# Performance work log

Hardware: AMD Instinct MI355X
Metric: run time of the kernel (lower is better)

## Reference

```python
import jax, jax.numpy as jnp
import numpy as np
from jax import lax

B, A, H, W = 64, 8, 64, 128
T_EXP = 32
ACTION_HORIZON = 64
DS = 1.0          # reward_cfg['ds']
TEMPERATURE = 0.1 # policy_kwargs['temperature'], method='sharpen'
FOV_HALF_ANGLE_DEG = 35.0
FOV_MAX_RANGE = 100


def _build_buffers():
    # per-action 3x3 one-hot transition kernels: weight 1.0 at 'center' cell,
    # 0.0 at left/right cells (as in MaxEntIRL.__init__ with policy_method='pp')
    center = [[2, 2], [2, 1], [2, 0], [1, 2], [1, 0], [0, 2], [0, 1], [0, 0]]
    tp = np.zeros((A, 1, 3, 3), np.float32)
    for i, (r, c) in enumerate(center):
        tp[i, 0, r, c] = 1.0
    # trapezoidal FOV mask built on a (2H, W) grid, then cropped to first H rows
    rows = np.arange(2 * H, dtype=np.float32)[:, None]
    cols = np.arange(W, dtype=np.float32)[None, :]
    half = np.tan(np.deg2rad(FOV_HALF_ANGLE_DEG)) * rows
    mask = ((np.abs(cols - (W - 1) / 2.0) <= half) & (rows <= FOV_MAX_RANGE))
    fov = mask.astype(np.float32)[:H][None, None]  # (1,1,H,W)
    dyn = np.array([[-1, -1], [-1, 0], [-1, 1], [0, -1],
                    [0, 1], [1, -1], [1, 0], [1, 1]], np.int32)
    return jnp.asarray(tp), jnp.asarray(fov), jnp.asarray(dyn)


def setup_inputs() -> dict:
    key = jax.random.key(0)
    k1, k2 = jax.random.split(key)
    policy = jax.random.normal(k1, (B, A, H, W), jnp.float32)
    # expert SE(2)-like poses; only [:, :, :2, 2] translations are read.
    # Scale to [0,100) so grid cells spread over the map before clamping.
    expert = jax.random.uniform(k2, (B, T_EXP, 3, 3), jnp.float32) * 100.0
    tp, fov, dyn = _build_buffers()
    return {"policy": policy, "expert": expert, "transition_probs": tp,
            "fov_mask": fov, "dynamics": dyn, "action_horizon": ACTION_HORIZON}


def reference(policy, expert, transition_probs, fov_mask, dynamics, action_horizon):
    Bn, An, Hn, Wn = policy.shape
    n_states = Hn * Wn
    barange = jnp.arange(Bn)

    # expert poses -> clamped grid cells  (S: (B, T, 2))
    S = jnp.floor_divide(expert[:, :, :2, 2], DS).astype(jnp.int32)
    S = jnp.stack([jnp.clip(S[..., 0], 0, Hn - 1),
                   jnp.clip(S[..., 1], 0, Wn - 1)], axis=-1)

    # earliest pose inside FOV (argmax of bool gives first True, else 0)
    mask2d = fov_mask[0, 0]
    in_fov = mask2d[S[..., 0], S[..., 1]] > 0  # (B, T)
    idx0 = jnp.argmax(in_fov, axis=1)
    S0c = S[barange, idx0]     # (B, 2) start cell
    S1c = S[:, -1]             # (B, 2) terminal cell
    S0 = S0c[:, 0] * Wn + S0c[:, 1]
    S1 = S1c[:, 0] * Wn + S1c[:, 1]

    # sharpen policy over action dim (stable softmax with temperature)
    logits = (policy - jnp.max(policy, axis=1, keepdims=True)) / TEMPERATURE
    policy_2d = jax.nn.softmax(logits, axis=1)  # (B, A, H, W)

    mu0 = jnp.zeros((Bn, n_states), jnp.float32).at[barange, S0].set(1.0)

    def step(carry, _):
        prev, total = carry
        # zero_terminal_state: kill visitation mass at the terminal cell
        prev_z = prev.at[barange, S1].set(0.0)
        pm = policy_2d * prev_z.reshape(Bn, 1, Hn, Wn)  # (B, A, H, W)
        new = lax.conv_general_dilated(
            pm, transition_probs, window_strides=(1, 1),
            padding=[(1, 1), (1, 1)],
            dimension_numbers=("NCHW", "OIHW", "NCHW"),
            feature_group_count=An)
        new = jnp.sum(new, axis=1).reshape(Bn, n_states)
        return (new, total + prev_z), None

    (last, total), _ = lax.scan(step, (mu0, jnp.zeros_like(mu0)),
                                None, length=action_horizon - 1)
    mu = (total + last).reshape(Bn, Hn, Wn)

    # greedy rollout (torch runs this under no_grad)
    policy_flat = policy.reshape(Bn, An, n_states)
    most_likely_action = jnp.argmax(policy_flat, axis=1)  # (B, n_states)
    most_likely_action = lax.stop_gradient(most_likely_action)

    def roll(St, _):
        a = most_likely_action[barange, St]
        coord = jnp.stack([St // Wn, St % Wn], axis=1) + dynamics[a]
        coord = jnp.stack([jnp.clip(coord[:, 0], 0, Hn - 1),
                           jnp.clip(coord[:, 1], 0, Wn - 1)], axis=1)
        return coord[:, 0] * Wn + coord[:, 1], coord

    _, coords = lax.scan(roll, S0, None, length=action_horizon - 1)  # (T-1,B,2)
    states = jnp.concatenate([S0c[None].astype(coords.dtype), coords],
                             axis=0).transpose(1, 0, 2)  # (B, T, 2)
    bidx = jnp.broadcast_to(barange[:, None], (Bn, action_horizon))
    states_grid = jnp.zeros((Bn, Hn, Wn), jnp.float32).at[
        bidx, states[..., 0], states[..., 1]].add(1.0)
    return mu, states_grid, states
```

## Files before the change

### kernel.cpp

```cpp
#include <hip/hip_runtime.h>

#define THREADS 1024

typedef unsigned int u32;
typedef unsigned long long u64;

constexpr int BN = 64, AN = 8, HN = 64, WN = 128;
constexpr int HWN = HN * WN;
constexpr int TEXP = 32, AH = 64;
constexpr size_t LDS_BYTES = (size_t)AN * HWN * 2;

constexpr int GYc[8] = { 1, 1, 1, 0, 0, -1, -1, -1 };
constexpr int GXc[8] = { 1, 0, -1, 1, -1, 1, 0, -1 };

typedef _Float16 h2 __attribute__((ext_vector_type(2)));
union U { u32 u; h2 p; _Float16 h[2]; };

__device__ __forceinline__ h2  H(u32 x) { U t; t.u = x; return t.p; }
__device__ __forceinline__ u32 Bc(h2 x) { U t; t.p = x; return t.u; }

__device__ __forceinline__ u32 ab16(u32 hi, u32 lo) {
    return (u32)((((u64)hi << 32) | lo) >> 16);
}
__device__ __forceinline__ u32 wsr1(u32 x) {
    return (u32)__builtin_amdgcn_update_dpp(0, (int)x, 0x138, 0xf, 0xf, true);
}
__device__ __forceinline__ u32 wsl1(u32 x) {
    return (u32)__builtin_amdgcn_update_dpp(0, (int)x, 0x130, 0xf, 0xf, true);
}
__device__ __forceinline__ u32 shL(u32 d) { return ab16(d, wsr1(d)); }
__device__ __forceinline__ u32 shR(u32 d) { return ab16(wsl1(d), d); }

extern "C" __global__ __launch_bounds__(THREADS)
void maxent_fused(const float* __restrict__ policy,
                  const float* __restrict__ expert,
                  const float* __restrict__ fovm,
                  const int*   __restrict__ dyn,
                  float* __restrict__ out)
{
    (void)dyn;
    extern __shared__ char smem[];
    const int tid  = threadIdx.x;
    const int lane = tid & 63;
    const bool isScan = blockIdx.x < BN;
    const int b = isScan ? (int)blockIdx.x : (int)blockIdx.x - BN;

    int Sr = 0, Sc = 0; bool infov = false;
    if (lane < TEXP) {
        float e0 = expert[b * (TEXP * 9) + lane * 9 + 2];
        float e1 = expert[b * (TEXP * 9) + lane * 9 + 5];
        int r = (int)floorf(e0); r = r < 0 ? 0 : (r > HN - 1 ? HN - 1 : r);
        int c = (int)floorf(e1); c = c < 0 ? 0 : (c > WN - 1 ? WN - 1 : c);
        Sr = r; Sc = c;
        infov = fovm[r * WN + c] > 0.0f;
    }
    unsigned long long fmask = __ballot(infov);
    int idx0 = fmask ? (__ffsll(fmask) - 1) : 0;
    const int S0r = __shfl(Sr, idx0), S0c = __shfl(Sc, idx0);
    const int S1r = __shfl(Sr, TEXP - 1), S1c = __shfl(Sc, TEXP - 1);
    const bool S0eqS1 = (S0r == S1r) && (S0c == S1c);

    if (isScan) {
        _Float16* Pl = (_Float16*)smem;

        const float* pb = policy + (size_t)b * AN * HWN;
        #pragma unroll
        for (int kk = 0; kk < 2; ++kk) {
            const int pix = (kk * THREADS + tid) * 4;
            float v[8][4];
            float m[4] = {-3.4e38f, -3.4e38f, -3.4e38f, -3.4e38f};
            #pragma unroll
            for (int a = 0; a < 8; ++a) {
                float4 f = *(const float4*)(pb + a * HWN + pix);
                v[a][0] = f.x; v[a][1] = f.y; v[a][2] = f.z; v[a][3] = f.w;
                m[0] = fmaxf(m[0], f.x); m[1] = fmaxf(m[1], f.y);
                m[2] = fmaxf(m[2], f.z); m[3] = fmaxf(m[3], f.w);
            }
            float s[4] = {0.f, 0.f, 0.f, 0.f};
            #pragma unroll
            for (int a = 0; a < 8; ++a)
                #pragma unroll
                for (int j = 0; j < 4; ++j) { v[a][j] = __expf((v[a][j] - m[j]) * 10.0f); s[j] += v[a][j]; }
            float inv[4];
            #pragma unroll
            for (int j = 0; j < 4; ++j) inv[j] = 1.0f / s[j];
            #pragma unroll
            for (int a = 0; a < 8; ++a) {
                u32 lo = (u32)__builtin_bit_cast(unsigned short, (_Float16)(v[a][0] * inv[0]))
                       | ((u32)__builtin_bit_cast(unsigned short, (_Float16)(v[a][1] * inv[1])) << 16);
                u32 hi = (u32)__builtin_bit_cast(unsigned short, (_Float16)(v[a][2] * inv[2]))
                       | ((u32)__builtin_bit_cast(unsigned short, (_Float16)(v[a][3] * inv[3])) << 16);
                uint2 pk2; pk2.x = lo; pk2.y = hi;
                *(uint2*)(Pl + a * HWN + pix) = pk2;
            }
        }
        __syncthreads();

        const int w = tid >> 6;
        const int rbase = 4 * w;

        u32 pa[8][4];
        #pragma unroll
        for (int a = 0; a < 8; ++a) {
            const int gy = GYc[a], gx = GXc[a];
            #pragma unroll
            for (int r = 0; r < 4; ++r) {
                const int sr = rbase + r + gy;
                u32 d = 0;
                if (sr >= 0 && sr < HN)
                    d = *(const u32*)(Pl + a * HWN + sr * WN + 2 * lane);
                pa[a][r] = (gx == 0) ? d : ((gx == 1) ? shR(d) : shL(d));
            }
        }
        __syncthreads();

        u32* hx = (u32*)smem;
        for (int i = tid; i < 4096; i += THREADS) hx[i] = 0;

        u32 x[6], zm[4];
        #pragma unroll
        for (int r = 0; r < 4; ++r) {
            const int gr = rbase + r;
            x[1 + r] = (!S0eqS1 && gr == S0r && (S0c >> 1) == lane)
                         ? ((S0c & 1) ? 0x3C000000u : 0x00003C00u) : 0u;
            zm[r] = ~0u;
            if (gr == S1r && (S1c >> 1) == lane)
                zm[r] = (S1c & 1) ? 0x0000FFFFu : 0xFFFF0000u;
        }
        x[0] = 0; x[5] = 0;
        __syncthreads();
        hx[(2 * w + 0) * 64 + lane] = x[1];
        hx[(2 * w + 1) * 64 + lane] = x[4];
        __syncthreads();

        u32 t16[4], nn[4];
        float tot[8];
        #pragma unroll
        for (int r = 0; r < 4; ++r) { t16[r] = 0; nn[r] = 0; }
        #pragma unroll
        for (int k = 0; k < 8; ++k) tot[k] = 0.f;

        const int rdT = (2 * w - 1) * 64 + lane;
        const int rdD = (2 * w + 2) * 64 + lane;
        const int wr0 = (2 * w + 0) * 64 + lane;
        const int wr3 = (2 * w + 1) * 64 + lane;

        for (int it = 0; it < AH - 1; ++it) {
            const int pb_ = (it & 1) << 11;
            const int wb_ = 2048 - pb_;
            const bool active = (rbase <= S0r + it + 1) && (rbase + 3 >= S0r - it - 1);
            if (active) {
                const u32 hT = (w > 0)  ? hx[pb_ + rdT] : 0u;
                const u32 hD = (w < 15) ? hx[pb_ + rdD] : 0u;

                #pragma unroll
                for (int r = 0; r < 4; ++r) t16[r] = Bc(H(t16[r]) + H(x[1 + r]));
                if ((it & 3) == 3 || it == AH - 2) {
                    #pragma unroll
                    for (int r = 0; r < 4; ++r) {
                        tot[2*r]   += (float)H(t16[r]).x;
                        tot[2*r+1] += (float)H(t16[r]).y;
                        t16[r] = 0;
                    }
                }

                u32 L[6], R[6];
                #pragma unroll
                for (int i = 1; i <= 4; ++i) { L[i] = shL(x[i]); R[i] = shR(x[i]); }

                u32 ns[4];
                constexpr int RO[4] = {1, 2, 0, 3};
                #pragma unroll
                for (int ri = 0; ri < 4; ++ri) {
                    const int r = RO[ri];
                    const u32 cm1 = (r == 0) ? hT      : x[r];
                    const u32 lm1 = (r == 0) ? shL(hT) : L[r];
                    const u32 rm1 = (r == 0) ? shR(hT) : R[r];
                    const u32 cp1 = (r == 3) ? hD      : x[r + 2];
                    const u32 lp1 = (r == 3) ? shL(hD) : L[r + 2];
                    const u32 rp1 = (r == 3) ? shR(hD) : R[r + 2];
                    h2 acc0 =  H(pa[0][r]) * H(rp1);
                    acc0 += H(pa[1][r]) * H(cp1);
                    acc0 += H(pa[2][r]) * H(lp1);
                    acc0 += H(pa[3][r]) * H(R[r + 1]);
                    h2 acc1 =  H(pa[4][r]) * H(L[r + 1]);
                    acc1 += H(pa[5][r]) * H(rm1);
                    acc1 += H(pa[6][r]) * H(cm1);
                    acc1 += H(pa[7][r]) * H(lm1);
                    const u32 un = Bc(acc0 + acc1);
                    nn[r] = un;
                    ns[r] = un & zm[r];
                }
                #pragma unroll
                for (int r = 0; r < 4; ++r) x[1 + r] = ns[r];

                hx[wb_ + wr0] = x[1];
                hx[wb_ + wr3] = x[4];
            }
            __syncthreads();
        }

        #pragma unroll
        for (int r = 0; r < 4; ++r) {
            float2 f;
            f.x = tot[2*r]   + (float)H(nn[r]).x;
            f.y = tot[2*r+1] + (float)H(nn[r]).y;
            *(float2*)(out + (size_t)b * HWN + (rbase + r) * WN + 2 * lane) = f;
        }

    } else {
        short* amap = (short*)smem;
        float* grid = (float*)(smem + 16384);
        const float* pb = policy + (size_t)b * AN * HWN;
        #pragma unroll
        for (int c = 0; c < 2; ++c) {
            const int pix = (c * THREADS + tid) * 4;
            float4 f0 = *(const float4*)(pb + pix);
            float b0 = f0.x, b1 = f0.y, b2 = f0.z, b3 = f0.w;
            int a0 = 0, a1 = 0, a2 = 0, a3 = 0;
            #pragma unroll
            for (int a = 1; a < 8; ++a) {
                float4 f = *(const float4*)(pb + a * HWN + pix);
                if (f.x > b0) { b0 = f.x; a0 = a; }
                if (f.y > b1) { b1 = f.y; a1 = a; }
                if (f.z > b2) { b2 = f.z; a2 = a; }
                if (f.w > b3) { b3 = f.w; a3 = a; }
            }
            uint2 pk2;
            pk2.x = (u32)a0 | ((u32)a1 << 16);
            pk2.y = (u32)a2 | ((u32)a3 << 16);
            *(uint2*)(amap + pix) = pk2;
        }
        for (int i = tid; i < HWN; i += THREADS) grid[i] = 0.f;
        __syncthreads();

        if (tid == 0) {
            float* so = out + 2 * (size_t)HWN * BN + b * (AH * 2);
            int cr = S0r, cc = S0c;
            so[0] = (float)cr; so[1] = (float)cc;
            grid[cr * WN + cc] += 1.0f;
            for (int t = 1; t < AH; ++t) {
                const int a = amap[cr * WN + cc];
                const int dr = (a < 3) ? -1 : ((a < 5) ? 0 : 1);
                int dc;
                if (a < 3) dc = a - 1;
                else if (a == 3) dc = -1;
                else if (a == 4) dc = 1;
                else dc = a - 6;
                cr += dr; cc += dc;
                cr = cr < 0 ? 0 : (cr > HN - 1 ? HN - 1 : cr);
                cc = cc < 0 ? 0 : (cc > WN - 1 ? WN - 1 : cc);
                so[t * 2] = (float)cr; so[t * 2 + 1] = (float)cc;
                grid[cr * WN + cc] += 1.0f;
            }
        }
        __syncthreads();
        float* sg = out + (size_t)HWN * BN + b * HWN;
        for (int i = tid; i < HWN; i += THREADS) sg[i] = grid[i];
    }
}

extern "C" void kernel_launch(void* const* d_in, const int* in_sizes, int n_in,
                              void* d_out, int out_size, void* d_ws, size_t ws_size,
                              hipStream_t stream) {
    const float* policy = (const float*)d_in[0];
    const float* expert = (const float*)d_in[1];
    const float* fovm   = (const float*)d_in[3];
    const int*   dyn    = (const int*)d_in[4];
    float* out = (float*)d_out;

    (void)hipFuncSetAttribute((const void*)maxent_fused,
                              hipFuncAttributeMaxDynamicSharedMemorySize,
                              (int)LDS_BYTES);
    hipLaunchKernelGGL(maxent_fused, dim3(2 * BN), dim3(THREADS), LDS_BYTES, stream,
                       policy, expert, fovm, dyn, out);
}
```

Measured before the change: 49.32 us.

## Split softmax/argmax prep into a wide kernel writing fp16 planes to workspace

Moves the per-pixel sharpened softmax and argmax out of the 128-block fused kernel into a separate 1024-block prep kernel. It writes packed fp16 probability planes and an argmax map to global workspace. The scan blocks then read their shifted neighbours straight from global memory instead of staging through LDS, which removes a barrier and shrinks LDS use. The aim is to spread the policy read and the exp work over the whole GPU instead of 128 blocks, at the cost of a second launch and an extra round trip through global memory (likely served from cache).

```diff
diff --git a/kernel.cpp b/kernel.cpp
--- a/kernel.cpp
+++ b/kernel.cpp
@@ -1,14 +1,14 @@
 #include <hip/hip_runtime.h>
 
-#define THREADS 1024
-
 typedef unsigned int u32;
+typedef unsigned short u16;
 typedef unsigned long long u64;
 
 constexpr int BN = 64, AN = 8, HN = 64, WN = 128;
 constexpr int HWN = HN * WN;
 constexpr int TEXP = 32, AH = 64;
-constexpr size_t LDS_BYTES = (size_t)AN * HWN * 2;
+constexpr size_t PLANES_U32 = (size_t)BN * AN * (HWN / 2);
+constexpr size_t LDS2 = 32768 + 2048;
 
 constexpr int GYc[8] = { 1, 1, 1, 0, 0, -1, -1, -1 };
 constexpr int GXc[8] = { 1, 0, -1, 1, -1, 1, 0, -1 };
@@ -31,14 +31,48 @@
 __device__ __forceinline__ u32 shL(u32 d) { return ab16(d, wsr1(d)); }
 __device__ __forceinline__ u32 shR(u32 d) { return ab16(wsl1(d), d); }
 
-extern "C" __global__ __launch_bounds__(THREADS)
-void maxent_fused(const float* __restrict__ policy,
-                  const float* __restrict__ expert,
+extern "C" __global__ __launch_bounds__(256)
+void prep_kernel(const float* __restrict__ policy, u32* __restrict__ planes,
+                 u32* __restrict__ amap)
+{
+    const int g = blockIdx.x * 256 + threadIdx.x;
+    const int b = g >> 12;
+    const int p = g & 4095;
+    const float* pb = policy + (size_t)b * AN * HWN + 2 * p;
+
+    float vx[8], vy[8];
+    float mx = -3.4e38f, my = -3.4e38f;
+    int ax = 0, ay = 0;
+    #pragma unroll
+    for (int a = 0; a < 8; ++a) {
+        float2 f = *(const float2*)(pb + a * HWN);
+        vx[a] = f.x; vy[a] = f.y;
+        if (f.x > mx) { mx = f.x; ax = a; }
+        if (f.y > my) { my = f.y; ay = a; }
+    }
+    float sx = 0.f, sy = 0.f;
+    #pragma unroll
+    for (int a = 0; a < 8; ++a) {
+        vx[a] = __expf((vx[a] - mx) * 10.0f); sx += vx[a];
+        vy[a] = __expf((vy[a] - my) * 10.0f); sy += vy[a];
+    }
+    const float ix = 1.0f / sx, iy = 1.0f / sy;
+    #pragma unroll
+    for (int a = 0; a < 8; ++a) {
+        u32 w = (u32)__builtin_bit_cast(u16, (_Float16)(vx[a] * ix))
+              | ((u32)__builtin_bit_cast(u16, (_Float16)(vy[a] * iy)) << 16);
+        planes[((size_t)(b * 8 + a) << 12) + p] = w;
+    }
+    amap[b * 4096 + p] = (u32)ax | ((u32)ay << 16);
+}
+
+extern "C" __global__ __launch_bounds__(1024)
+void maxent_fused(const float* __restrict__ expert,
                   const float* __restrict__ fovm,
-                  const int*   __restrict__ dyn,
+                  const u32* __restrict__ planes,
+                  const u16* __restrict__ gmap,
                   float* __restrict__ out)
 {
-    (void)dyn;
     extern __shared__ char smem[];
     const int tid  = threadIdx.x;
     const int lane = tid & 63;
@@ -61,41 +95,6 @@
     const bool S0eqS1 = (S0r == S1r) && (S0c == S1c);
 
     if (isScan) {
-        _Float16* Pl = (_Float16*)smem;
-
-        const float* pb = policy + (size_t)b * AN * HWN;
-        #pragma unroll
-        for (int kk = 0; kk < 2; ++kk) {
-            const int pix = (kk * THREADS + tid) * 4;
-            float v[8][4];
-            float m[4] = {-3.4e38f, -3.4e38f, -3.4e38f, -3.4e38f};
-            #pragma unroll
-            for (int a = 0; a < 8; ++a) {
-                float4 f = *(const float4*)(pb + a * HWN + pix);
-                v[a][0] = f.x; v[a][1] = f.y; v[a][2] = f.z; v[a][3] = f.w;
-                m[0] = fmaxf(m[0], f.x); m[1] = fmaxf(m[1], f.y);
-                m[2] = fmaxf(m[2], f.z); m[3] = fmaxf(m[3], f.w);
-            }
-            float s[4] = {0.f, 0.f, 0.f, 0.f};
-            #pragma unroll
-            for (int a = 0; a < 8; ++a)
-                #pragma unroll
-                for (int j = 0; j < 4; ++j) { v[a][j] = __expf((v[a][j] - m[j]) * 10.0f); s[j] += v[a][j]; }
-            float inv[4];
-            #pragma unroll
-            for (int j = 0; j < 4; ++j) inv[j] = 1.0f / s[j];
-            #pragma unroll
-            for (int a = 0; a < 8; ++a) {
-                u32 lo = (u32)__builtin_bit_cast(unsigned short, (_Float16)(v[a][0] * inv[0]))
-                       | ((u32)__builtin_bit_cast(unsigned short, (_Float16)(v[a][1] * inv[1])) << 16);
-                u32 hi = (u32)__builtin_bit_cast(unsigned short, (_Float16)(v[a][2] * inv[2]))
-                       | ((u32)__builtin_bit_cast(unsigned short, (_Float16)(v[a][3] * inv[3])) << 16);
-                uint2 pk2; pk2.x = lo; pk2.y = hi;
-                *(uint2*)(Pl + a * HWN + pix) = pk2;
-            }
-        }
-        __syncthreads();
-
         const int w = tid >> 6;
         const int rbase = 4 * w;
 
@@ -103,19 +102,18 @@
         #pragma unroll
         for (int a = 0; a < 8; ++a) {
             const int gy = GYc[a], gx = GXc[a];
+            const u32* pl = planes + ((size_t)(b * 8 + a) << 12);
             #pragma unroll
             for (int r = 0; r < 4; ++r) {
                 const int sr = rbase + r + gy;
                 u32 d = 0;
-                if (sr >= 0 && sr < HN)
-                    d = *(const u32*)(Pl + a * HWN + sr * WN + 2 * lane);
+                if (sr >= 0 && sr < HN) d = pl[(sr << 6) + lane];
                 pa[a][r] = (gx == 0) ? d : ((gx == 1) ? shR(d) : shL(d));
             }
         }
-        __syncthreads();
 
         u32* hx = (u32*)smem;
-        for (int i = tid; i < 4096; i += THREADS) hx[i] = 0;
+        for (int i = tid; i < 4096; i += 1024) hx[i] = 0;
 
         u32 x[6], zm[4];
         #pragma unroll
@@ -209,38 +207,18 @@
         }
 
     } else {
-        short* amap = (short*)smem;
-        float* grid = (float*)(smem + 16384);
-        const float* pb = policy + (size_t)b * AN * HWN;
-        #pragma unroll
-        for (int c = 0; c < 2; ++c) {
-            const int pix = (c * THREADS + tid) * 4;
-            float4 f0 = *(const float4*)(pb + pix);
-            float b0 = f0.x, b1 = f0.y, b2 = f0.z, b3 = f0.w;
-            int a0 = 0, a1 = 0, a2 = 0, a3 = 0;
-            #pragma unroll
-            for (int a = 1; a < 8; ++a) {
-                float4 f = *(const float4*)(pb + a * HWN + pix);
-                if (f.x > b0) { b0 = f.x; a0 = a; }
-                if (f.y > b1) { b1 = f.y; a1 = a; }
-                if (f.z > b2) { b2 = f.z; a2 = a; }
-                if (f.w > b3) { b3 = f.w; a3 = a; }
-            }
-            uint2 pk2;
-            pk2.x = (u32)a0 | ((u32)a1 << 16);
-            pk2.y = (u32)a2 | ((u32)a3 << 16);
-            *(uint2*)(amap + pix) = pk2;
-        }
-        for (int i = tid; i < HWN; i += THREADS) grid[i] = 0.f;
+        float* grid = (float*)smem;
+        for (int i = tid; i < HWN; i += 1024) grid[i] = 0.f;
         __syncthreads();
 
         if (tid == 0) {
+            const u16* am = gmap + (size_t)b * HWN;
             float* so = out + 2 * (size_t)HWN * BN + b * (AH * 2);
             int cr = S0r, cc = S0c;
             so[0] = (float)cr; so[1] = (float)cc;
             grid[cr * WN + cc] += 1.0f;
             for (int t = 1; t < AH; ++t) {
-                const int a = amap[cr * WN + cc];
+                const int a = am[cr * WN + cc];
                 const int dr = (a < 3) ? -1 : ((a < 5) ? 0 : 1);
                 int dc;
                 if (a < 3) dc = a - 1;
@@ -256,7 +234,7 @@
         }
         __syncthreads();
         float* sg = out + (size_t)HWN * BN + b * HWN;
-        for (int i = tid; i < HWN; i += THREADS) sg[i] = grid[i];
+        for (int i = tid; i < HWN; i += 1024) sg[i] = grid[i];
     }
 }
 
@@ -266,12 +244,14 @@
     const float* policy = (const float*)d_in[0];
     const float* expert = (const float*)d_in[1];
     const float* fovm   = (const float*)d_in[3];
-    const int*   dyn    = (const int*)d_in[4];
     float* out = (float*)d_out;
 
-    (void)hipFuncSetAttribute((const void*)maxent_fused,
-                              hipFuncAttributeMaxDynamicSharedMemorySize,
-                              (int)LDS_BYTES);
-    hipLaunchKernelGGL(maxent_fused, dim3(2 * BN), dim3(THREADS), LDS_BYTES, stream,
-                       policy, expert, fovm, dyn, out);
-}
+    u32* planes = (u32*)d_ws;
+    u32* amap32 = planes + PLANES_U32;
+    const u16* gmap = (const u16*)amap32;
+
+    hipLaunchKernelGGL(prep_kernel, dim3(1024), dim3(256), 0, stream,
+                       policy, planes, amap32);
+    hipLaunchKernelGGL(maxent_fused, dim3(2 * BN), dim3(1024), LDS2, stream,
+                       expert, fovm, planes, gmap, out);
+}
```

Measured after the change: 52.68 us (median of 4 runs). +6.8%, slower.

## Fuse two propagation steps per barrier using two-row ghost halos

Applied to the files above, without the earlier changes.

The stencil propagation loop now advances two time steps per iteration. Each wave keeps a 6-row register window, with policy weights extended to 6 rows, and exchanges two halo rows per side through LDS. This halves the number of __syncthreads barriers and LDS round-trips across the 63-step horizon. In exchange it does redundant stencil work on the halo rows, raises register pressure (pa grows to 8x6), and doubles the LDS exchange buffer.

```diff
diff --git a/kernel.cpp b/kernel.cpp
--- a/kernel.cpp
+++ b/kernel.cpp
@@ -3,6 +3,7 @@
 #define THREADS 1024
 
 typedef unsigned int u32;
+typedef unsigned short u16;
 typedef unsigned long long u64;
 
 constexpr int BN = 64, AN = 8, HN = 64, WN = 128;
@@ -30,6 +31,13 @@
 }
 __device__ __forceinline__ u32 shL(u32 d) { return ab16(d, wsr1(d)); }
 __device__ __forceinline__ u32 shR(u32 d) { return ab16(wsl1(d), d); }
+
+#define STEN(J, sm1, Lm1, Rm1, s0, L0, R0, sp1, Lp1, Rp1, OUTV)            \
+{ h2 a0 = H(pa[0][J]) * H(Rp1); a0 += H(pa[1][J]) * H(sp1);                \
+  a0 += H(pa[2][J]) * H(Lp1);   a0 += H(pa[3][J]) * H(R0);                 \
+  h2 a1 = H(pa[4][J]) * H(L0);  a1 += H(pa[5][J]) * H(Rm1);                \
+  a1 += H(pa[6][J]) * H(sm1);   a1 += H(pa[7][J]) * H(Lm1);                \
+  OUTV = Bc(a0 + a1); }
 
 extern "C" __global__ __launch_bounds__(THREADS)
 void maxent_fused(const float* __restrict__ policy,
@@ -86,10 +94,10 @@
             for (int j = 0; j < 4; ++j) inv[j] = 1.0f / s[j];
             #pragma unroll
             for (int a = 0; a < 8; ++a) {
-                u32 lo = (u32)__builtin_bit_cast(unsigned short, (_Float16)(v[a][0] * inv[0]))
-                       | ((u32)__builtin_bit_cast(unsigned short, (_Float16)(v[a][1] * inv[1])) << 16);
-                u32 hi = (u32)__builtin_bit_cast(unsigned short, (_Float16)(v[a][2] * inv[2]))
-                       | ((u32)__builtin_bit_cast(unsigned short, (_Float16)(v[a][3] * inv[3])) << 16);
+                u32 lo = (u32)__builtin_bit_cast(u16, (_Float16)(v[a][0] * inv[0]))
+                       | ((u32)__builtin_bit_cast(u16, (_Float16)(v[a][1] * inv[1])) << 16);
+                u32 hi = (u32)__builtin_bit_cast(u16, (_Float16)(v[a][2] * inv[2]))
+                       | ((u32)__builtin_bit_cast(u16, (_Float16)(v[a][3] * inv[3])) << 16);
                 uint2 pk2; pk2.x = lo; pk2.y = hi;
                 *(uint2*)(Pl + a * HWN + pix) = pk2;
             }
@@ -99,38 +107,43 @@
         const int w = tid >> 6;
         const int rbase = 4 * w;
 
-        u32 pa[8][4];
+        u32 pa[8][6];
         #pragma unroll
         for (int a = 0; a < 8; ++a) {
             const int gy = GYc[a], gx = GXc[a];
             #pragma unroll
-            for (int r = 0; r < 4; ++r) {
-                const int sr = rbase + r + gy;
+            for (int j = 0; j < 6; ++j) {
+                const int sr = rbase - 1 + j + gy;
                 u32 d = 0;
                 if (sr >= 0 && sr < HN)
                     d = *(const u32*)(Pl + a * HWN + sr * WN + 2 * lane);
-                pa[a][r] = (gx == 0) ? d : ((gx == 1) ? shR(d) : shL(d));
+                pa[a][j] = (gx == 0) ? d : ((gx == 1) ? shR(d) : shL(d));
             }
         }
         __syncthreads();
 
         u32* hx = (u32*)smem;
-        for (int i = tid; i < 4096; i += THREADS) hx[i] = 0;
-
-        u32 x[6], zm[4];
+        for (int i = tid; i < 8192; i += THREADS) hx[i] = 0;
+
+        u32 x[8], zm6[6];
+        #pragma unroll
+        for (int j = 0; j < 6; ++j) {
+            const int gr = rbase - 1 + j;
+            zm6[j] = ~0u;
+            if (gr == S1r && (S1c >> 1) == lane)
+                zm6[j] = (S1c & 1) ? 0x0000FFFFu : 0xFFFF0000u;
+        }
         #pragma unroll
         for (int r = 0; r < 4; ++r) {
             const int gr = rbase + r;
-            x[1 + r] = (!S0eqS1 && gr == S0r && (S0c >> 1) == lane)
+            x[2 + r] = (!S0eqS1 && gr == S0r && (S0c >> 1) == lane)
                          ? ((S0c & 1) ? 0x3C000000u : 0x00003C00u) : 0u;
-            zm[r] = ~0u;
-            if (gr == S1r && (S1c >> 1) == lane)
-                zm[r] = (S1c & 1) ? 0x0000FFFFu : 0xFFFF0000u;
-        }
-        x[0] = 0; x[5] = 0;
-        __syncthreads();
-        hx[(2 * w + 0) * 64 + lane] = x[1];
-        hx[(2 * w + 1) * 64 + lane] = x[4];
+        }
+        x[0] = 0; x[1] = 0; x[6] = 0; x[7] = 0;
+        __syncthreads();
+        #pragma unroll
+        for (int j = 0; j < 4; ++j)
+            hx[w * 256 + j * 64 + lane] = x[2 + j];
         __syncthreads();
 
         u32 t16[4], nn[4];
@@ -140,64 +153,82 @@
         #pragma unroll
         for (int k = 0; k < 8; ++k) tot[k] = 0.f;
 
-        const int rdT = (2 * w - 1) * 64 + lane;
-        const int rdD = (2 * w + 2) * 64 + lane;
-        const int wr0 = (2 * w + 0) * 64 + lane;
-        const int wr3 = (2 * w + 1) * 64 + lane;
-
-        for (int it = 0; it < AH - 1; ++it) {
-            const int pb_ = (it & 1) << 11;
-            const int wb_ = 2048 - pb_;
-            const bool active = (rbase <= S0r + it + 1) && (rbase + 3 >= S0r - it - 1);
+        const int rT2 = (w - 1) * 256 + 2 * 64 + lane;
+        const int rT1 = (w - 1) * 256 + 3 * 64 + lane;
+        const int rD0 = (w + 1) * 256 + 0 * 64 + lane;
+        const int rD1 = (w + 1) * 256 + 1 * 64 + lane;
+        const int wbase = w * 256 + lane;
+
+        for (int p = 0; p < 31; ++p) {
+            const int it = 2 * p;
+            const int rd = (p & 1) << 12;
+            const int wb = 4096 - rd;
+            const bool active = (rbase <= S0r + it + 3) && (rbase + 3 >= S0r - it - 3);
             if (active) {
-                const u32 hT = (w > 0)  ? hx[pb_ + rdT] : 0u;
-                const u32 hD = (w < 15) ? hx[pb_ + rdD] : 0u;
-
-                #pragma unroll
-                for (int r = 0; r < 4; ++r) t16[r] = Bc(H(t16[r]) + H(x[1 + r]));
-                if ((it & 3) == 3 || it == AH - 2) {
-                    #pragma unroll
-                    for (int r = 0; r < 4; ++r) {
-                        tot[2*r]   += (float)H(t16[r]).x;
-                        tot[2*r+1] += (float)H(t16[r]).y;
-                        t16[r] = 0;
-                    }
+                x[0] = (w > 0)  ? hx[rd + rT2] : 0u;
+                x[1] = (w > 0)  ? hx[rd + rT1] : 0u;
+                x[6] = (w < 15) ? hx[rd + rD0] : 0u;
+                x[7] = (w < 15) ? hx[rd + rD1] : 0u;
+
+                #pragma unroll
+                for (int r = 0; r < 4; ++r) t16[r] = Bc(H(t16[r]) + H(x[2 + r]));
+
+                u32 L[8], R[8], y[6];
+                #pragma unroll
+                for (int i = 0; i < 8; ++i) { L[i] = shL(x[i]); R[i] = shR(x[i]); }
+                #pragma unroll
+                for (int j = 0; j < 6; ++j) {
+                    STEN(j, x[j], L[j], R[j], x[j+1], L[j+1], R[j+1],
+                         x[j+2], L[j+2], R[j+2], y[j]);
+                    y[j] &= zm6[j];
                 }
-
-                u32 L[6], R[6];
-                #pragma unroll
-                for (int i = 1; i <= 4; ++i) { L[i] = shL(x[i]); R[i] = shR(x[i]); }
-
-                u32 ns[4];
-                constexpr int RO[4] = {1, 2, 0, 3};
-                #pragma unroll
-                for (int ri = 0; ri < 4; ++ri) {
-                    const int r = RO[ri];
-                    const u32 cm1 = (r == 0) ? hT      : x[r];
-                    const u32 lm1 = (r == 0) ? shL(hT) : L[r];
-                    const u32 rm1 = (r == 0) ? shR(hT) : R[r];
-                    const u32 cp1 = (r == 3) ? hD      : x[r + 2];
-                    const u32 lp1 = (r == 3) ? shL(hD) : L[r + 2];
-                    const u32 rp1 = (r == 3) ? shR(hD) : R[r + 2];
-                    h2 acc0 =  H(pa[0][r]) * H(rp1);
-                    acc0 += H(pa[1][r]) * H(cp1);
-                    acc0 += H(pa[2][r]) * H(lp1);
-                    acc0 += H(pa[3][r]) * H(R[r + 1]);
-                    h2 acc1 =  H(pa[4][r]) * H(L[r + 1]);
-                    acc1 += H(pa[5][r]) * H(rm1);
-                    acc1 += H(pa[6][r]) * H(cm1);
-                    acc1 += H(pa[7][r]) * H(lm1);
-                    const u32 un = Bc(acc0 + acc1);
-                    nn[r] = un;
-                    ns[r] = un & zm[r];
+                #pragma unroll
+                for (int r = 0; r < 4; ++r) t16[r] = Bc(H(t16[r]) + H(y[1 + r]));
+
+                #pragma unroll
+                for (int i = 0; i < 6; ++i) { L[i] = shL(y[i]); R[i] = shR(y[i]); }
+                #pragma unroll
+                for (int m = 0; m < 4; ++m) {
+                    u32 un;
+                    STEN(m + 1, y[m], L[m], R[m], y[m+1], L[m+1], R[m+1],
+                         y[m+2], L[m+2], R[m+2], un);
+                    x[2 + m] = un & zm6[m + 1];
                 }
-                #pragma unroll
-                for (int r = 0; r < 4; ++r) x[1 + r] = ns[r];
-
-                hx[wb_ + wr0] = x[1];
-                hx[wb_ + wr3] = x[4];
+
+                #pragma unroll
+                for (int j = 0; j < 4; ++j)
+                    hx[wb + wbase + j * 64] = x[2 + j];
+            }
+            if (p & 1) {
+                #pragma unroll
+                for (int r = 0; r < 4; ++r) {
+                    tot[2*r]   += (float)H(t16[r]).x;
+                    tot[2*r+1] += (float)H(t16[r]).y;
+                    t16[r] = 0;
+                }
             }
             __syncthreads();
+        }
+
+        {
+            const int rd = (31 & 1) << 12;
+            x[1] = (w > 0)  ? hx[rd + rT1] : 0u;
+            x[6] = (w < 15) ? hx[rd + rD0] : 0u;
+            #pragma unroll
+            for (int r = 0; r < 4; ++r) t16[r] = Bc(H(t16[r]) + H(x[2 + r]));
+            u32 L[7], R[7];
+            #pragma unroll
+            for (int i = 1; i <= 6; ++i) { L[i] = shL(x[i]); R[i] = shR(x[i]); }
+            #pragma unroll
+            for (int m = 0; m < 4; ++m) {
+                STEN(m + 1, x[m+1], L[m+1], R[m+1], x[m+2], L[m+2], R[m+2],
+                     x[m+3], L[m+3], R[m+3], nn[m]);
+            }
+            #pragma unroll
+            for (int r = 0; r < 4; ++r) {
+                tot[2*r]   += (float)H(t16[r]).x;
+                tot[2*r+1] += (float)H(t16[r]).y;
+            }
         }
 
         #pragma unroll
```

Result: slower. 50.65 us (+2.7%).
